# Kernel tuning notes

Measured on AMD Instinct MI355X. Metric: run time of the kernel, lower is better.

## Reference

```python
import jax, jax.numpy as jnp
import numpy as np

EPS = 1e-6
NUM_HEADS = 12


def ln_cf(x, w, b):
    # channels_first LayerNorm over channel dim (ConvNeXt style)
    u = jnp.mean(x, axis=1, keepdims=True)
    s = jnp.mean((x - u) ** 2, axis=1, keepdims=True)
    xn = (x - u) / jnp.sqrt(s + EPS)
    shp = (1, -1) + (1,) * (x.ndim - 2)
    return xn * w.reshape(shp) + b.reshape(shp)


def conv2s2(x, w):
    # Conv3d kernel=2 stride=2 (no bias): exact non-overlapping patch contraction
    b, c, H, W, D = x.shape
    xp = x.reshape(b, c, H // 2, 2, W // 2, 2, D // 2, 2)
    return jnp.einsum('bchkwpdq,ockpq->bohwd', xp, w)


def convt2s2(x, w):
    # ConvTranspose3d kernel=2 stride=2 (torch weight layout [in, out, 2,2,2])
    b, i, H, W, D = x.shape
    o = w.shape[1]
    y = jnp.einsum('bihwd,iokpq->bohkwpdq', x, w)
    return y.reshape(b, o, 2 * H, 2 * W, 2 * D)


def stem(x, w1, g1, b1, w2, g2, b2):
    h = conv2s2(x, w1)
    h = jax.nn.gelu(ln_cf(h, g1, b1), approximate=False)
    h = conv2s2(h, w2)
    return ln_cf(h, g2, b2)


def debed(x, tw1, g, b, tw2, tb2):
    h = convt2s2(x, tw1)
    h = jax.nn.gelu(ln_cf(h, g, b), approximate=False)
    return convt2s2(h, tw2) + tb2.reshape(1, -1, 1, 1, 1)


def rope(x):
    # rotary embedding over full token dim c (pairs (i, i+c/2)), positions 0..L-1
    b, l, c = x.shape
    inv = 1.0 / (10000.0 ** (jnp.arange(0, c, 2, dtype=jnp.float32) / c))
    t = jnp.arange(l, dtype=jnp.float32)
    f = jnp.outer(t, inv)                      # [l, c/2]
    emb = jnp.concatenate([f, f], axis=-1)     # [l, c]
    cos, sin = jnp.cos(emb)[None], jnp.sin(emb)[None]
    rot = jnp.concatenate([-x[..., c // 2:], x[..., :c // 2]], axis=-1)
    return x * cos + rot * sin


def _forward(x, skip, q_w1, q_g1, q_b1, q_w2, q_g2, q_b2,
             k_w1, k_g1, k_b1, k_w2, k_g2, k_b2,
             v_w1, v_g1, v_b1, v_w2, v_g2, v_b2,
             o_tw1, o_g, o_b, o_tw2, o_tb2,
             ns_w, ns_b, nx_w, nx_b, no_w, no_b):
    res = skip
    skip = ln_cf(skip, ns_w, ns_b)
    x = ln_cf(x, nx_w, nx_b)
    q = stem(skip, q_w1, q_g1, q_b1, q_w2, q_g2, q_b2)
    k = stem(x, k_w1, k_g1, k_b1, k_w2, k_g2, k_b2)
    v = stem(x, v_w1, v_g1, v_b1, v_w2, v_g2, v_b2)
    b, c, Hq, Wq, Dq = q.shape
    _, _, Hk, Wk, Dk = k.shape
    q = q.reshape(b, c, -1).transpose(0, 2, 1)   # [b, Lq, c]
    k = k.reshape(b, c, -1).transpose(0, 2, 1)   # [b, Lk, c]
    v = v.reshape(b, c, -1).transpose(0, 2, 1)
    q = rope(q)
    k = rope(k)
    hd = c // NUM_HEADS
    qh = q.reshape(b, -1, NUM_HEADS, hd).transpose(0, 2, 1, 3)  # [b, nh, Lq, hd]
    kh = k.reshape(b, -1, NUM_HEADS, hd).transpose(0, 2, 1, 3)
    vh = v.reshape(b, -1, NUM_HEADS, hd).transpose(0, 2, 1, 3)
    scale = 1.0 / jnp.sqrt(jnp.float32(hd))
    attn = jax.nn.softmax(jnp.einsum('bhqc,bhkc->bhqk', qh, kh) * scale, axis=-1)
    proj = jnp.einsum('bhqk,bhkc->bhqc', attn, vh)              # [b, nh, Lq, hd]
    # rearrange 'b nh l c -> b (c nh) h w d'
    proj = proj.transpose(0, 3, 1, 2).reshape(b, c, Hq, Wq, Dq)
    proj = ln_cf(proj, no_w, no_b)
    out = debed(proj, o_tw1, o_g, o_b, o_tw2, o_tb2)
    return out + res


def setup_inputs() -> dict:
    key = jax.random.key(0)
    ks = iter(jax.random.split(key, 40))
    def nrm(shape, scale):
        return jax.random.normal(next(ks), shape, jnp.float32) * scale
    E, E4, XF, SF = 768, 192, 6, 6
    inp = {
        'x': nrm((2, XF, 48, 48, 48), 1.0),
        'skip': nrm((2, SF, 48, 48, 48), 1.0),
    }
    for p, ic in [('q', SF), ('k', XF), ('v', XF)]:
        inp[p + '_w1'] = nrm((E4, ic, 2, 2, 2), (ic * 8) ** -0.5)
        inp[p + '_g1'] = jnp.ones(E4, jnp.float32)
        inp[p + '_b1'] = jnp.zeros(E4, jnp.float32)
        inp[p + '_w2'] = nrm((E, E4, 2, 2, 2), (E4 * 8) ** -0.5)
        inp[p + '_g2'] = jnp.ones(E, jnp.float32)
        inp[p + '_b2'] = jnp.zeros(E, jnp.float32)
    inp['o_tw1'] = nrm((E, E4, 2, 2, 2), E ** -0.5)
    inp['o_g'] = jnp.ones(E4, jnp.float32)
    inp['o_b'] = jnp.zeros(E4, jnp.float32)
    inp['o_tw2'] = nrm((E4, SF, 2, 2, 2), E4 ** -0.5)
    inp['o_tb2'] = jnp.zeros(SF, jnp.float32)
    inp['ns_w'] = jnp.ones(SF, jnp.float32)
    inp['ns_b'] = jnp.zeros(SF, jnp.float32)
    inp['nx_w'] = jnp.ones(XF, jnp.float32)
    inp['nx_b'] = jnp.zeros(XF, jnp.float32)
    inp['no_w'] = jnp.ones(E, jnp.float32)
    inp['no_b'] = jnp.zeros(E, jnp.float32)
    return inp


def reference(x, skip, q_w1, q_g1, q_b1, q_w2, q_g2, q_b2,
              k_w1, k_g1, k_b1, k_w2, k_g2, k_b2,
              v_w1, v_g1, v_b1, v_w2, v_g2, v_b2,
              o_tw1, o_g, o_b, o_tw2, o_tb2,
              ns_w, ns_b, nx_w, nx_b, no_w, no_b):
    return _forward(x, skip, q_w1, q_g1, q_b1, q_w2, q_g2, q_b2,
                    k_w1, k_g1, k_b1, k_w2, k_g2, k_b2,
                    v_w1, v_g1, v_b1, v_w2, v_g2, v_b2,
                    o_tw1, o_g, o_b, o_tw2, o_tb2,
                    ns_w, ns_b, nx_w, nx_b, no_w, no_b)
```

## Files before the change

### kernel.cpp

```cpp
#include <hip/hip_runtime.h>
#include <math.h>

#define BB_ 2
#define C0 6
#define S0 48
#define V0 (S0*S0*S0)
#define C1 192
#define S1 24
#define V1 (S1*S1*S1)
#define C2 768
#define S2 12
#define LL (S2*S2*S2)
#define NH 12
#define HD 64
#define KDIM (C1*8)
#define MDIM (BB_*LL)

typedef __attribute__((ext_vector_type(8))) short short8;
typedef __attribute__((ext_vector_type(4))) short short4v;
typedef __attribute__((ext_vector_type(4))) float float4v;

static __device__ __forceinline__ float gelu_exact(float x){
  return 0.5f*x*(1.0f+erff(x*0.70710678118654752440f));
}
static __device__ __forceinline__ unsigned short f2bf(float f){
  unsigned int u = __float_as_uint(f);
  unsigned int r = (u + 0x7fffu + ((u>>16)&1u)) >> 16;
  return (unsigned short)r;
}
static __device__ __forceinline__ unsigned int pk_bf16(float a, float b){
#if __has_builtin(__builtin_amdgcn_cvt_pk_bf16_f32)
  typedef __attribute__((ext_vector_type(2))) __bf16 bf2;
  bf2 r = __builtin_amdgcn_cvt_pk_bf16_f32(a,b);
  union { bf2 v; unsigned int u; } cv; cv.v = r;
  return cv.u;
#else
  return (unsigned int)f2bf(a) | ((unsigned int)f2bf(b)<<16);
#endif
}
static __device__ __forceinline__ float bf2f(unsigned short u){
  return __uint_as_float(((unsigned int)u)<<16);
}
static __device__ __forceinline__ void load_lds16(const void* g, void* l){
  __builtin_amdgcn_global_load_lds((const __attribute__((address_space(1))) unsigned int*)g,
      (__attribute__((address_space(3))) unsigned int*)l, 16, 0, 0);
}
static __device__ __forceinline__ float4v mfma32(short8 a, short8 b, float4v c){
  return __builtin_amdgcn_mfma_f32_16x16x32_bf16(a,b,c,0,0,0);
}
static __device__ __forceinline__ float4v mfma16(short4v a, short4v b, float4v c){
#if __has_builtin(__builtin_amdgcn_mfma_f32_16x16x16bf16_1k)
  return __builtin_amdgcn_mfma_f32_16x16x16bf16_1k(a,b,c,0,0,0);
#else
  asm volatile("v_mfma_f32_16x16x16_bf16 %0, %1, %2, %0" : "+v"(c) : "v"(a), "v"(b));
  return c;
#endif
}

__global__ __launch_bounds__(256) void prep_kernel(
    const float* __restrict__ skin, const float* __restrict__ xin,
    const float* __restrict__ nsw, const float* __restrict__ nsb,
    const float* __restrict__ nxw, const float* __restrict__ nxb,
    unsigned short* __restrict__ outS, unsigned short* __restrict__ outX,
    const float* __restrict__ qw2, const float* __restrict__ kw2, const float* __restrict__ vw2,
    const float* __restrict__ tw1, const float* __restrict__ tw2,
    unsigned short* __restrict__ w2tq, unsigned short* __restrict__ w2tk,
    unsigned short* __restrict__ w2tv, unsigned short* __restrict__ Btd,
    unsigned short* __restrict__ Bt48){
  int bx = blockIdx.x;
  if (bx < 1728){
    int z = bx >= 864;
    const float* in = z ? xin : skin;
    const float* w  = z ? nxw : nsw;
    const float* bi = z ? nxb : nsb;
    unsigned short* out = z ? outX : outS;
    int idx = (bx - z*864)*256 + threadIdx.x;
    int b = idx / V0, vox = idx - b*V0;
    const float* p = in + (size_t)b*(C0*V0) + vox;
    float v[C0]; float s=0.f;
#pragma unroll
    for (int c=0;c<C0;c++){ v[c]=p[(size_t)c*V0]; s+=v[c]; }
    float u = s*(1.f/C0);
    float ss=0.f;
#pragma unroll
    for (int c=0;c<C0;c++){ float d=v[c]-u; ss+=d*d; }
    float inv = rsqrtf(ss*(1.f/C0)+1e-6f);
    unsigned short* o = out + (size_t)b*(C0*V0) + vox;
#pragma unroll
    for (int c=0;c<C0;c++) o[(size_t)c*V0] = f2bf((v[c]-u)*inv*w[c]+bi[c]);
    return;
  }
  bx -= 1728;
  if (bx < 13824){
    int z = bx/4608;
    int idx = (bx - z*4608)*256 + threadIdx.x;
    const float* w2 = (z==0)?qw2:((z==1)?kw2:vw2);
    unsigned short* o = (z==0)?w2tq:((z==1)?w2tk:w2tv);
    int oc = idx/KDIM; int r = idx-oc*KDIM; int p = r/C1; int ic = r-p*C1;
    o[idx] = f2bf(w2[(size_t)oc*KDIM + ic*8 + p]);
  } else if (bx < 18432){
    int idx = (bx-13824)*256 + threadIdx.x;
    int n = idx/C2; int p = idx-n*C2;
    int i = ((p&63)*NH) + (p>>6);
    int kpq = n/C1, o2 = n-kpq*C1;
    Btd[idx] = f2bf(tw1[(size_t)i*KDIM + o2*8 + kpq]);
  } else {
    int idx = (bx-18432)*256 + threadIdx.x;
    int n = idx/C1; int i = idx-n*C1;
    Bt48[idx] = (n<48) ? f2bf(tw2[(size_t)i*48 + n]) : (unsigned short)0;
  }
}

__global__ __launch_bounds__(256) void conv1_kernel(
    const unsigned short* __restrict__ lnSb, const unsigned short* __restrict__ lnXb,
    const float* __restrict__ qw1, const float* __restrict__ qg1, const float* __restrict__ qb1,
    const float* __restrict__ kw1, const float* __restrict__ kg1, const float* __restrict__ kb1,
    const float* __restrict__ vw1, const float* __restrict__ vg1, const float* __restrict__ vb1,
    unsigned short* __restrict__ h1q, unsigned short* __restrict__ h1k,
    unsigned short* __restrict__ h1v){
  int z = blockIdx.z;
  const unsigned short* in = (z==0)? lnSb : lnXb;
  const float* w1 = (z==0)?qw1:((z==1)?kw1:vw1);
  const float* g1 = (z==0)?qg1:((z==1)?kg1:vg1);
  const float* b1 = (z==0)?qb1:((z==1)?kb1:vb1);
  unsigned short* h1p = (z==0)?h1q:((z==1)?h1k:h1v);
  __shared__ unsigned short Wl[C1*56];
  __shared__ float Gl[C1], Bl2[C1];
  int t = threadIdx.x, w = t>>6, lane = t&63;
  int g = lane>>4, l16 = lane&15;
  int j = blockIdx.x*4 + w;
  int bxh = j/18, mt = j - bxh*18;
  int b = bxh/48; int rem = bxh - b*48; int y = rem>>1, xh = rem&1;
  int xo = mt/3, zo = mt - xo*3;
  int xv = xh*12 + xo*2 + (l16>>3);
  int zv = zo*8 + (l16&7);
  int x2 = 2*xv, z2 = 2*zv, y2 = 2*y;
  const unsigned short* base = in + (size_t)b*C0*V0;
  union { short8 v; unsigned int u[4]; } aA;
  {
    size_t rb = (size_t)g*V0;
    aA.u[0] = *(const unsigned int*)&base[rb + (y2+0)*(S0*S0) + (x2+0)*S0 + z2];
    aA.u[1] = *(const unsigned int*)&base[rb + (y2+0)*(S0*S0) + (x2+1)*S0 + z2];
    aA.u[2] = *(const unsigned int*)&base[rb + (y2+1)*(S0*S0) + (x2+0)*S0 + z2];
    aA.u[3] = *(const unsigned int*)&base[rb + (y2+1)*(S0*S0) + (x2+1)*S0 + z2];
  }
  union { short4v v; unsigned int u[2]; } aB;
  {
    size_t rb = (size_t)(4+(g>>1))*V0 + (y2+(g&1))*(S0*S0);
    aB.u[0] = *(const unsigned int*)&base[rb + (x2+0)*S0 + z2];
    aB.u[1] = *(const unsigned int*)&base[rb + (x2+1)*S0 + z2];
  }
  for (int i4 = t; i4 < 2304; i4 += 256){
    int oc = i4/12, kk4 = (i4 - oc*12)*4;
    float4 f4 = *(const float4*)&w1[oc*48 + kk4];
    uint2 pk; pk.x = pk_bf16(f4.x,f4.y); pk.y = pk_bf16(f4.z,f4.w);
    *(uint2*)&Wl[oc*56 + kk4] = pk;
  }
  if (t < C1){ Gl[t] = g1[t]; Bl2[t] = b1[t]; }
  __syncthreads();
  float4v acc[12];
#pragma unroll
  for (int ot=0; ot<12; ot++){
    short8  wA = *(const short8*)&Wl[(ot*16+l16)*56 + g*8];
    short4v wB = *(const short4v*)&Wl[(ot*16+l16)*56 + 32 + g*4];
    float4v a = {};
    a = mfma32(wA, aA.v, a);
    a = mfma16(wB, aB.v, a);
    acc[ot] = a;
  }
  float s1=0.f, s2=0.f;
#pragma unroll
  for (int ot=0;ot<12;ot++)
#pragma unroll
    for (int reg=0;reg<4;reg++){ float v=acc[ot][reg]; s1+=v; s2+=v*v; }
  s1 += __shfl_xor(s1,16); s1 += __shfl_xor(s1,32);
  s2 += __shfl_xor(s2,16); s2 += __shfl_xor(s2,32);
  float u = s1*(1.f/C1);
  float inv = rsqrtf(s2*(1.f/C1)-u*u+1e-6f);
  int tok = (y>>1)*(S2*S2) + (xv>>1)*S2 + (zv>>1);
  int p8 = (y&1)*4 + (xv&1)*2 + (zv&1);
  unsigned short* hb = h1p + (size_t)(b*LL+tok)*KDIM + p8*C1;
#pragma unroll
  for (int ot=0; ot<12; ot++){
    int oc0 = ot*16 + g*4;
    float4 gg = *(const float4*)&Gl[oc0];
    float4 bb = *(const float4*)&Bl2[oc0];
    float x0 = gelu_exact((acc[ot][0]-u)*inv*gg.x+bb.x);
    float x1 = gelu_exact((acc[ot][1]-u)*inv*gg.y+bb.y);
    float x2e= gelu_exact((acc[ot][2]-u)*inv*gg.z+bb.z);
    float x3 = gelu_exact((acc[ot][3]-u)*inv*gg.w+bb.w);
    uint2 pk; pk.x = pk_bf16(x0,x1); pk.y = pk_bf16(x2e,x3);
    *(uint2*)&hb[oc0] = pk;
  }
}

__global__ __launch_bounds__(256) void gemm_stem_kernel(
    const unsigned short* __restrict__ A0, const unsigned short* __restrict__ A1,
    const unsigned short* __restrict__ A2,
    const unsigned short* __restrict__ B0, const unsigned short* __restrict__ B1,
    const unsigned short* __restrict__ B2,
    unsigned short* __restrict__ Cq, unsigned short* __restrict__ Ck,
    unsigned short* __restrict__ Cv){
  int flat = blockIdx.x;
  int xcd = flat & 7, slot = flat >> 3;
  int tile = xcd*61 + slot;
  if (tile >= 486) return;
  int z = tile/162; int rr = tile - z*162;
  int m0 = (rr/6)*128, n0 = (rr - (rr/6)*6)*128;
  const unsigned short* A = (z==0)?A0:((z==1)?A1:A2);
  const unsigned short* Bt = (z==0)?B0:((z==1)?B1:B2);
  unsigned short* Cp = (z==0)?Cq:((z==1)?Ck:Cv);
  __shared__ __align__(16) unsigned short Al[128*32];
  __shared__ __align__(16) unsigned short Bl[128*32];
  int t=threadIdx.x, w=t>>6, lane=t&63;
  int g=lane>>4, l16=lane&15, r16=lane>>2, c16=lane&3;
  int wm=w>>1, wn=w&1;
  float4v acc[4][4] = {};
  for (int kb=0;kb<KDIM;kb+=32){
    __syncthreads();
#pragma unroll
    for (int cc=0;cc<4;cc++){
      int ch = w*4+cc;
      if (ch<8){
        const unsigned short* gp = A + (size_t)(m0+ch*16+r16)*KDIM + kb + c16*8;
        load_lds16(gp, &Al[ch*512]);
      } else {
        const unsigned short* gp = Bt + (size_t)(n0+(ch-8)*16+r16)*KDIM + kb + c16*8;
        load_lds16(gp, &Bl[(ch-8)*512]);
      }
    }
    __syncthreads();
    short8 af[4], bf[4];
#pragma unroll
    for (int mt=0;mt<4;mt++) af[mt] = *(const short8*)&Al[(wm*64+mt*16+l16)*32 + g*8];
#pragma unroll
    for (int nt=0;nt<4;nt++) bf[nt] = *(const short8*)&Bl[(wn*64+nt*16+l16)*32 + g*8];
#pragma unroll
    for (int mt=0;mt<4;mt++)
#pragma unroll
      for (int nt=0;nt<4;nt++)
        acc[mt][nt] = mfma32(af[mt], bf[nt], acc[mt][nt]);
  }
#pragma unroll
  for (int mt=0;mt<4;mt++){
    int mb = m0 + wm*64 + mt*16 + g*4;
#pragma unroll
    for (int nt=0;nt<4;nt++){
      int col = n0 + wn*64 + nt*16 + l16;
#pragma unroll
      for (int reg=0;reg<4;reg++)
        Cp[(size_t)(mb+reg)*C2 + col] = f2bf(acc[mt][nt][reg]);
    }
  }
}

__global__ __launch_bounds__(256) void gemm_debed_kernel(const unsigned short* __restrict__ A,
    const unsigned short* __restrict__ Bt, unsigned short* __restrict__ C){
  int flat = blockIdx.x;
  int xcd = flat & 7, slot = flat >> 3;
  int tile = xcd*41 + slot;
  if (tile >= 324) return;
  int m0 = (tile/12)*128, n0 = (tile - (tile/12)*12)*128;
  __shared__ __align__(16) unsigned short Al[128*32];
  __shared__ __align__(16) unsigned short Bl[128*32];
  int t=threadIdx.x, w=t>>6, lane=t&63;
  int g=lane>>4, l16=lane&15, r16=lane>>2, c16=lane&3;
  int wm=w>>1, wn=w&1;
  float4v acc[4][4] = {};
  for (int kb=0;kb<C2;kb+=32){
    __syncthreads();
#pragma unroll
    for (int cc=0;cc<4;cc++){
      int ch = w*4+cc;
      if (ch<8){
        const unsigned short* gp = A + (size_t)(m0+ch*16+r16)*C2 + kb + c16*8;
        load_lds16(gp, &Al[ch*512]);
      } else {
        const unsigned short* gp = Bt + (size_t)(n0+(ch-8)*16+r16)*C2 + kb + c16*8;
        load_lds16(gp, &Bl[(ch-8)*512]);
      }
    }
    __syncthreads();
    short8 af[4], bf[4];
#pragma unroll
    for (int mt=0;mt<4;mt++) af[mt] = *(const short8*)&Al[(wm*64+mt*16+l16)*32 + g*8];
#pragma unroll
    for (int nt=0;nt<4;nt++) bf[nt] = *(const short8*)&Bl[(wn*64+nt*16+l16)*32 + g*8];
#pragma unroll
    for (int mt=0;mt<4;mt++)
#pragma unroll
      for (int nt=0;nt<4;nt++)
        acc[mt][nt] = mfma32(af[mt], bf[nt], acc[mt][nt]);
  }
#pragma unroll
  for (int nt=0;nt<4;nt++){
    int n = n0 + wn*64 + nt*16 + l16;
    int kpq = n / C1;
    int o = n - kpq*C1;
#pragma unroll
    for (int mt=0;mt<4;mt++){
      int mb = m0 + wm*64 + mt*16 + g*4;
#pragma unroll
      for (int reg=0;reg<4;reg++){
        int m = mb + reg;
        int b = m / LL; int tok = m - b*LL;
        int h = tok/(S2*S2), ww=(tok/S2)%S2, d=tok%S2;
        int v24 = (2*h+((kpq>>2)&1))*(S1*S1) + (2*ww+((kpq>>1)&1))*S1 + (2*d+(kpq&1));
        C[(size_t)(b*V1+v24)*C1 + o] = f2bf(acc[mt][nt][reg]);
      }
    }
  }
}

__global__ __launch_bounds__(256) void final_kernel(const unsigned short* __restrict__ dh,
    const unsigned short* __restrict__ Bt48, const float* __restrict__ og,
    const float* __restrict__ ob, const float* __restrict__ tb2s,
    const float* __restrict__ skipp, float* __restrict__ out){
  __shared__ __align__(16) unsigned short As[64*200];
  __shared__ __align__(16) unsigned short Bs[64*200];
  int t=threadIdx.x, w=t>>6, lane=t&63;
  int g=lane>>4, l16=lane&15;
  int m0 = blockIdx.x*64;
  for (int n8 = t; n8 < 1536; n8 += 256){
    int n64 = n8/24, kk = (n8 - n64*24)*8;
    uint4 d4 = *(const uint4*)&Bt48[n64*192 + kk];
    *(uint4*)&Bs[n64*200 + kk] = d4;
  }
  float g0=og[lane], g1v=og[lane+64], g2v=og[lane+128];
  float b0=ob[lane], b1v=ob[lane+64], b2v=ob[lane+128];
  for (int rr=0; rr<16; rr++){
    int rl = w*16 + rr;
    const unsigned short* row = dh + (size_t)(m0+rl)*C1;
    float v0=bf2f(row[lane]), v1=bf2f(row[lane+64]), v2=bf2f(row[lane+128]);
    float s1=v0+v1+v2, s2=v0*v0+v1*v1+v2*v2;
#pragma unroll
    for (int off=32;off>0;off>>=1){ s1+=__shfl_xor(s1,off); s2+=__shfl_xor(s2,off); }
    float u=s1*(1.f/C1), inv=rsqrtf(s2*(1.f/C1)-u*u+1e-6f);
    As[rl*200+lane]     = f2bf(gelu_exact((v0-u)*inv*g0+b0));
    As[rl*200+lane+64]  = f2bf(gelu_exact((v1-u)*inv*g1v+b1v));
    As[rl*200+lane+128] = f2bf(gelu_exact((v2-u)*inv*g2v+b2v));
  }
  __syncthreads();
  int wm=w>>1, wn=w&1;
  float4v acc[2][2] = {};
#pragma unroll
  for (int kb=0;kb<192;kb+=32){
    short8 af[2], bf[2];
#pragma unroll
    for (int mt=0;mt<2;mt++) af[mt] = *(const short8*)&As[(wm*32+mt*16+l16)*200 + kb + g*8];
#pragma unroll
    for (int nt=0;nt<2;nt++) bf[nt] = *(const short8*)&Bs[(wn*32+nt*16+l16)*200 + kb + g*8];
#pragma unroll
    for (int mt=0;mt<2;mt++)
#pragma unroll
      for (int nt=0;nt<2;nt++)
        acc[mt][nt] = mfma32(af[mt], bf[nt], acc[mt][nt]);
  }
#pragma unroll
  for (int nt=0;nt<2;nt++){
    int n = wn*32 + nt*16 + l16;
    if (n < 48){
      int c = n>>3, kpq = n&7;
      float bias = tb2s[c];
#pragma unroll
      for (int mt=0;mt<2;mt++){
        int mb = m0 + wm*32 + mt*16 + g*4;
#pragma unroll
        for (int reg=0;reg<4;reg++){
          int m = mb + reg;
          int b = m / V1; int v24 = m - b*V1;
          int y24 = v24/(S1*S1), x24=(v24/S1)%S1, z24=v24%S1;
          int vox = (2*y24+((kpq>>2)&1))*(S0*S0) + (2*x24+((kpq>>1)&1))*S0 + 2*z24+(kpq&1);
          size_t oi = (size_t)(b*C0+c)*V0 + vox;
          out[oi] = acc[mt][nt][reg] + bias + skipp[oi];
        }
      }
    }
  }
}

__global__ __launch_bounds__(64) void ln768_stem_kernel(
    unsigned short* __restrict__ qb, unsigned short* __restrict__ kb2,
    unsigned short* __restrict__ vb,
    const float* __restrict__ qg, const float* __restrict__ qbi,
    const float* __restrict__ kg, const float* __restrict__ kbi,
    const float* __restrict__ vg, const float* __restrict__ vbi, float qscale){
  int z = blockIdx.y;
  unsigned short* buf = (z==0)?qb:((z==1)?kb2:vb);
  const float* g  = (z==0)?qg:((z==1)?kg:vg);
  const float* bia= (z==0)?qbi:((z==1)?kbi:vbi);
  float scale = (z==0)? qscale : 1.0f;
  int tok = blockIdx.x, lane = threadIdx.x;
  unsigned short* row = buf + (size_t)tok*C2;
  float v[12]; float s1=0.f,s2=0.f;
#pragma unroll
  for (int i=0;i<12;i++){ float t=bf2f(row[i*64+lane]); v[i]=t; s1+=t; s2+=t*t; }
#pragma unroll
  for (int off=32;off>0;off>>=1){ s1+=__shfl_xor(s1,off); s2+=__shfl_xor(s2,off); }
  float u=s1*(1.f/C2);
  float inv=rsqrtf(s2*(1.f/C2)-u*u+1e-6f);
  if (z==2){
#pragma unroll
    for (int i=0;i<12;i++){ int j=i*64+lane; row[j]=f2bf((v[i]-u)*inv*g[j]+bia[j]); }
  } else {
    int pos = tok % LL;
#pragma unroll
    for (int i=0;i<6;i++){
      int j=i*64+lane;
      float xn1=(v[i]-u)*inv*g[j]+bia[j];
      float xn2=(v[i+6]-u)*inv*g[j+384]+bia[j+384];
      float fr=(float)pos*__expf(-0.02398526139f*(float)j);
      float cs=cosf(fr), sn=sinf(fr);
      row[j]     = f2bf((xn1*cs - xn2*sn)*scale);
      row[j+384] = f2bf((xn2*cs + xn1*sn)*scale);
    }
  }
}

__global__ __launch_bounds__(256) void vtrans_kernel(const unsigned short* __restrict__ vbf,
    unsigned short* __restrict__ vT){
  int idx = blockIdx.x*256 + threadIdx.x;
  int token = idx % LL;
  int rest = idx / LL;
  int dc = rest & 7;
  int hb = rest >> 3;
  int h = hb % NH, b = hb / NH;
  const unsigned short* src = vbf + (size_t)(b*LL+token)*C2 + h*64 + dc*8;
  uint4 d4 = *(const uint4*)src;
  const unsigned short* s = (const unsigned short*)&d4;
#pragma unroll
  for (int i=0;i<8;i++)
    vT[(size_t)((b*NH+h)*HD + dc*8 + i)*LL + token] = s[i];
}

__global__ __launch_bounds__(256) void attn_kernel(const unsigned short* __restrict__ q,
    const unsigned short* __restrict__ k, const unsigned short* __restrict__ vt,
    unsigned short* __restrict__ opart, float* __restrict__ lbuf){
  __shared__ __align__(16) unsigned char smem[18432];
  unsigned short* Ks = (unsigned short*)smem;
  unsigned short* Vs = Ks + 4096;
  int qt=blockIdx.x, h=blockIdx.y;
  int b = blockIdx.z>>2, split = blockIdx.z&3;
  int t=threadIdx.x, w=t>>6, lane=t&63;
  int g=lane>>4, l16=lane&15;
  const unsigned short* qrow = q + (size_t)(b*LL + qt*64 + w*16 + l16)*C2 + h*64;
  short8 qA = *(const short8*)(qrow + g*8);
  short8 qB = *(const short8*)(qrow + 32 + g*8);
  const unsigned short* kbase = k + (size_t)(b*LL)*C2 + h*64;
  const unsigned short* vbase = vt + (size_t)((b*NH+h)*HD)*LL;
  int sub = lane>>3;
  int chs = (lane&7) ^ sub;
  float lrow = 0.f;
  float4v O4[4] = {};
  int ktb = split*7, kte = (split==3)? 27 : (split*7+7);
  for (int kt=ktb; kt<kte; kt++){
    __syncthreads();
#pragma unroll
    for (int cc=0;cc<4;cc++){
      int ii = w*4+cc;
      if (ii<8){
        int key = kt*64 + ii*8 + sub;
        load_lds16(kbase + (size_t)key*C2 + chs*8, &Ks[ii*512]);
      } else {
        int d = (ii-8)*8 + sub;
        load_lds16(vbase + (size_t)d*LL + kt*64 + chs*8, &Vs[(ii-8)*512]);
      }
    }
    __syncthreads();
    float4v sc[4];
#pragma unroll
    for (int nt=0;nt<4;nt++){
      int row = nt*16 + l16;
      int sw = row & 7;
      short8 k1 = *(const short8*)&Ks[row*64 + ((g^sw))*8];
      short8 k2 = *(const short8*)&Ks[row*64 + (((4+g)^sw))*8];
      float4v z = {};
      z = mfma32(k1, qA, z);
      z = mfma32(k2, qB, z);
      sc[nt] = z;
    }
#pragma unroll
    for (int nt=0;nt<4;nt++)
#pragma unroll
      for (int reg=0;reg<4;reg++){
        float e = exp2f(sc[nt][reg]); sc[nt][reg]=e; lrow+=e;
      }
#pragma unroll
    for (int kc=0;kc<4;kc++){
      union { short4v v; unsigned int u[2]; } pb;
      pb.u[0] = pk_bf16(sc[kc][0], sc[kc][1]);
      pb.u[1] = pk_bf16(sc[kc][2], sc[kc][3]);
#pragma unroll
      for (int dt=0;dt<4;dt++){
        int row = dt*16 + l16;
        int ch = (kc*2 + (g>>1)) ^ (row&7);
        short4v va = *(const short4v*)&Vs[row*64 + ch*8 + (g&1)*4];
        O4[dt] = mfma16(va, pb.v, O4[dt]);
      }
    }
  }
  lrow += __shfl_xor(lrow,16);
  lrow += __shfl_xor(lrow,32);
  __syncthreads();
  float* Ot = (float*)smem;
  float* ot = Ot + w*1152;
#pragma unroll
  for (int dt=0;dt<4;dt++)
    *(float4*)&ot[l16*72 + dt*16 + g*4] =
        make_float4(O4[dt][0],O4[dt][1],O4[dt][2],O4[dt][3]);
  if (g==0){
    int qi = qt*64 + w*16 + l16;
    lbuf[((size_t)(b*4+split)*NH+h)*LL + qi] = lrow;
  }
  int qq = lane>>2, c4 = lane&3;
  unsigned short* orow = opart + (size_t)split*MDIM*C2
              + (size_t)(b*LL + qt*64 + w*16 + qq)*C2 + h*64;
#pragma unroll
  for (int p=0;p<4;p++){
    float4 vv = *(float4*)&ot[qq*72 + p*16 + c4*4];
    uint2 pk; pk.x = pk_bf16(vv.x,vv.y); pk.y = pk_bf16(vv.z,vv.w);
    *(uint2*)&orow[p*16 + c4*4] = pk;
  }
}

__global__ __launch_bounds__(256) void attn_post_kernel(const unsigned short* __restrict__ opart,
    const float* __restrict__ lbuf,
    const float* __restrict__ g, const float* __restrict__ bia,
    unsigned short* __restrict__ aob){
  int t=threadIdx.x, w=t>>6, lane=t&63;
  int m = blockIdx.x*4 + w;
  int b = m / LL, l = m - b*LL;
  const unsigned short* o0 = opart + (size_t)m*C2;
  unsigned short* orow = aob + (size_t)m*C2;
  float vv[12]; float s1=0.f, s2=0.f;
#pragma unroll
  for (int i=0;i<12;i++){
    float ls = 0.f;
#pragma unroll
    for (int s=0;s<4;s++) ls += lbuf[((size_t)(b*4+s)*NH+i)*LL + l];
    float inv = 1.f/ls;
    int j = i*64+lane;
    float val = 0.f;
#pragma unroll
    for (int s=0;s<4;s++) val += bf2f(o0[(size_t)s*MDIM*C2 + j]);
    val *= inv;
    vv[i]=val; s1+=val; s2+=val*val;
  }
#pragma unroll
  for (int off=32;off>0;off>>=1){ s1+=__shfl_xor(s1,off); s2+=__shfl_xor(s2,off); }
  float u=s1*(1.f/C2);
  float invs=rsqrtf(s2*(1.f/C2)-u*u+1e-6f);
#pragma unroll
  for (int i=0;i<12;i++){
    int cj = lane*NH + i;
    orow[i*64+lane] = f2bf((vv[i]-u)*invs*g[cj]+bia[cj]);
  }
}

extern "C" void kernel_launch(void* const* d_in, const int* in_sizes, int n_in,
                              void* d_out, int out_size, void* d_ws, size_t ws_size,
                              hipStream_t stream){
  (void)in_sizes; (void)n_in; (void)out_size; (void)ws_size;
  const float* x    =(const float*)d_in[0];
  const float* skip =(const float*)d_in[1];
  const float* q_w1 =(const float*)d_in[2];
  const float* q_g1 =(const float*)d_in[3];
  const float* q_b1 =(const float*)d_in[4];
  const float* q_w2 =(const float*)d_in[5];
  const float* q_g2 =(const float*)d_in[6];
  const float* q_b2 =(const float*)d_in[7];
  const float* k_w1 =(const float*)d_in[8];
  const float* k_g1 =(const float*)d_in[9];
  const float* k_b1 =(const float*)d_in[10];
  const float* k_w2 =(const float*)d_in[11];
  const float* k_g2 =(const float*)d_in[12];
  const float* k_b2 =(const float*)d_in[13];
  const float* v_w1 =(const float*)d_in[14];
  const float* v_g1 =(const float*)d_in[15];
  const float* v_b1 =(const float*)d_in[16];
  const float* v_w2 =(const float*)d_in[17];
  const float* v_g2 =(const float*)d_in[18];
  const float* v_b2 =(const float*)d_in[19];
  const float* o_tw1=(const float*)d_in[20];
  const float* o_g  =(const float*)d_in[21];
  const float* o_b  =(const float*)d_in[22];
  const float* o_tw2=(const float*)d_in[23];
  const float* o_tb2=(const float*)d_in[24];
  const float* ns_w =(const float*)d_in[25];
  const float* ns_b =(const float*)d_in[26];
  const float* nx_w =(const float*)d_in[27];
  const float* nx_b =(const float*)d_in[28];
  const float* no_w =(const float*)d_in[29];
  const float* no_b =(const float*)d_in[30];
  float* out=(float*)d_out;

  char* W = (char*)d_ws;
  unsigned short* lnSb = (unsigned short*)(W + 0);
  unsigned short* lnXb = (unsigned short*)(W + 2654208);
  unsigned short* h1q  = (unsigned short*)(W + 5308416);
  unsigned short* h1k  = (unsigned short*)(W + 15925248);
  unsigned short* h1v  = (unsigned short*)(W + 26542080);
  unsigned short* w2tq = (unsigned short*)(W + 37158912);
  unsigned short* w2tk = (unsigned short*)(W + 39518208);
  unsigned short* w2tv = (unsigned short*)(W + 41877504);
  unsigned short* qbf  = (unsigned short*)(W + 44236800);
  unsigned short* kbf  = (unsigned short*)(W + 49545216);
  unsigned short* vbf  = (unsigned short*)(W + 54853632);
  unsigned short* vT   = (unsigned short*)(W + 60162048);
  unsigned short* aob  = (unsigned short*)(W + 65470464);
  unsigned short* Btd  = (unsigned short*)(W + 70778880);
  unsigned short* Bt48 = (unsigned short*)(W + 73138176);
  float* lbuf  = (float*)(W + 0);
  unsigned short* opart = (unsigned short*)(W + 5308416);
  unsigned short* dh   = (unsigned short*)(W + 5308416);

  const float QSCALE = 0.125f*1.44269504089f;

  prep_kernel<<<20208,256,0,stream>>>(skip, x, ns_w, ns_b, nx_w, nx_b, lnSb, lnXb,
      q_w2,k_w2,v_w2,o_tw1,o_tw2, w2tq,w2tk,w2tv,Btd,Bt48);
  conv1_kernel<<<dim3(432,1,3),256,0,stream>>>(lnSb,lnXb,
      q_w1,q_g1,q_b1, k_w1,k_g1,k_b1, v_w1,v_g1,v_b1, h1q,h1k,h1v);
  gemm_stem_kernel<<<488,256,0,stream>>>(h1q,h1k,h1v,
      w2tq,w2tk,w2tv, qbf,kbf,vbf);
  ln768_stem_kernel<<<dim3(MDIM,3),64,0,stream>>>(qbf,kbf,vbf,
      q_g2,q_b2, k_g2,k_b2, v_g2,v_b2, QSCALE);
  vtrans_kernel<<<1296,256,0,stream>>>(vbf, vT);
  attn_kernel<<<dim3(27,12,8),256,0,stream>>>(qbf, kbf, vT, opart, lbuf);
  attn_post_kernel<<<864,256,0,stream>>>(opart, lbuf, no_w, no_b, aob);
  gemm_debed_kernel<<<328,256,0,stream>>>(aob, Btd, dh);
  final_kernel<<<432,256,0,stream>>>(dh, Bt48, o_g, o_b, o_tb2, skip, out);
}
```

Before: 334.8 us.

## Pre-convert conv1 weights in prep, XCD-remap attention grid, MFMA row sums

Conv1 weights are now converted to bf16 once in the prep kernel, and conv1 reads them and the LN params straight from global memory, which drops the shared-memory staging and its barrier. The attention grid is flattened and remapped so tiles sharing a head land on the same XCD, aiming for better L2 reuse of K/V. The softmax row sum is computed by an extra MFMA against a ones vector instead of per-element adds and shuffles, taking the work off the VALU. The trade-offs are uncached global weight loads in conv1 and a row sum built from bf16-rounded probabilities.

Result: no change. 329.0 us (-1.7%).

```diff
diff --git a/kernel.cpp b/kernel.cpp
--- a/kernel.cpp
+++ b/kernel.cpp
@@ -64,9 +64,12 @@
     unsigned short* __restrict__ outS, unsigned short* __restrict__ outX,
     const float* __restrict__ qw2, const float* __restrict__ kw2, const float* __restrict__ vw2,
     const float* __restrict__ tw1, const float* __restrict__ tw2,
+    const float* __restrict__ qw1, const float* __restrict__ kw1, const float* __restrict__ vw1,
     unsigned short* __restrict__ w2tq, unsigned short* __restrict__ w2tk,
     unsigned short* __restrict__ w2tv, unsigned short* __restrict__ Btd,
-    unsigned short* __restrict__ Bt48){
+    unsigned short* __restrict__ Bt48,
+    unsigned short* __restrict__ w1q, unsigned short* __restrict__ w1k,
+    unsigned short* __restrict__ w1v){
   int bx = blockIdx.x;
   if (bx < 1728){
     int z = bx >= 864;
@@ -104,28 +107,34 @@
     int i = ((p&63)*NH) + (p>>6);
     int kpq = n/C1, o2 = n-kpq*C1;
     Btd[idx] = f2bf(tw1[(size_t)i*KDIM + o2*8 + kpq]);
-  } else {
+  } else if (bx < 18480){
     int idx = (bx-18432)*256 + threadIdx.x;
     int n = idx/C1; int i = idx-n*C1;
     Bt48[idx] = (n<48) ? f2bf(tw2[(size_t)i*48 + n]) : (unsigned short)0;
+  } else {
+    int idx = (bx-18480)*256 + threadIdx.x;
+    int z = idx / 9216; int r = idx - z*9216;
+    const float* w1 = (z==0)?qw1:((z==1)?kw1:vw1);
+    unsigned short* o = (z==0)?w1q:((z==1)?w1k:w1v);
+    o[r] = f2bf(w1[r]);
   }
 }
 
 __global__ __launch_bounds__(256) void conv1_kernel(
     const unsigned short* __restrict__ lnSb, const unsigned short* __restrict__ lnXb,
-    const float* __restrict__ qw1, const float* __restrict__ qg1, const float* __restrict__ qb1,
-    const float* __restrict__ kw1, const float* __restrict__ kg1, const float* __restrict__ kb1,
-    const float* __restrict__ vw1, const float* __restrict__ vg1, const float* __restrict__ vb1,
+    const unsigned short* __restrict__ w1bq, const unsigned short* __restrict__ w1bk,
+    const unsigned short* __restrict__ w1bv,
+    const float* __restrict__ qg1, const float* __restrict__ qb1,
+    const float* __restrict__ kg1, const float* __restrict__ kb1,
+    const float* __restrict__ vg1, const float* __restrict__ vb1,
     unsigned short* __restrict__ h1q, unsigned short* __restrict__ h1k,
     unsigned short* __restrict__ h1v){
   int z = blockIdx.z;
   const unsigned short* in = (z==0)? lnSb : lnXb;
-  const float* w1 = (z==0)?qw1:((z==1)?kw1:vw1);
+  const unsigned short* Wb = (z==0)?w1bq:((z==1)?w1bk:w1bv);
   const float* g1 = (z==0)?qg1:((z==1)?kg1:vg1);
   const float* b1 = (z==0)?qb1:((z==1)?kb1:vb1);
   unsigned short* h1p = (z==0)?h1q:((z==1)?h1k:h1v);
-  __shared__ unsigned short Wl[C1*56];
-  __shared__ float Gl[C1], Bl2[C1];
   int t = threadIdx.x, w = t>>6, lane = t&63;
   int g = lane>>4, l16 = lane&15;
   int j = blockIdx.x*4 + w;
@@ -150,19 +159,11 @@
     aB.u[0] = *(const unsigned int*)&base[rb + (x2+0)*S0 + z2];
     aB.u[1] = *(const unsigned int*)&base[rb + (x2+1)*S0 + z2];
   }
-  for (int i4 = t; i4 < 2304; i4 += 256){
-    int oc = i4/12, kk4 = (i4 - oc*12)*4;
-    float4 f4 = *(const float4*)&w1[oc*48 + kk4];
-    uint2 pk; pk.x = pk_bf16(f4.x,f4.y); pk.y = pk_bf16(f4.z,f4.w);
-    *(uint2*)&Wl[oc*56 + kk4] = pk;
-  }
-  if (t < C1){ Gl[t] = g1[t]; Bl2[t] = b1[t]; }
-  __syncthreads();
   float4v acc[12];
 #pragma unroll
   for (int ot=0; ot<12; ot++){
-    short8  wA = *(const short8*)&Wl[(ot*16+l16)*56 + g*8];
-    short4v wB = *(const short4v*)&Wl[(ot*16+l16)*56 + 32 + g*4];
+    short8  wA = *(const short8*)&Wb[(ot*16+l16)*48 + g*8];
+    short4v wB = *(const short4v*)&Wb[(ot*16+l16)*48 + 32 + g*4];
     float4v a = {};
     a = mfma32(wA, aA.v, a);
     a = mfma16(wB, aB.v, a);
@@ -183,8 +184,8 @@
 #pragma unroll
   for (int ot=0; ot<12; ot++){
     int oc0 = ot*16 + g*4;
-    float4 gg = *(const float4*)&Gl[oc0];
-    float4 bb = *(const float4*)&Bl2[oc0];
+    float4 gg = *(const float4*)&g1[oc0];
+    float4 bb = *(const float4*)&b1[oc0];
     float x0 = gelu_exact((acc[ot][0]-u)*inv*gg.x+bb.x);
     float x1 = gelu_exact((acc[ot][1]-u)*inv*gg.y+bb.y);
     float x2e= gelu_exact((acc[ot][2]-u)*inv*gg.z+bb.z);
@@ -439,8 +440,12 @@
   __shared__ __align__(16) unsigned char smem[18432];
   unsigned short* Ks = (unsigned short*)smem;
   unsigned short* Vs = Ks + 4096;
-  int qt=blockIdx.x, h=blockIdx.y;
-  int b = blockIdx.z>>2, split = blockIdx.z&3;
+  int flat = blockIdx.x;
+  int xcd = flat & 7, slot = flat >> 3;
+  int tile = xcd*324 + slot;
+  int h = tile / 216; int rem = tile - h*216;
+  int zb = rem / 27, qt = rem - zb*27;
+  int b = zb >> 2, split = zb & 3;
   int t=threadIdx.x, w=t>>6, lane=t&63;
   int g=lane>>4, l16=lane&15;
   const unsigned short* qrow = q + (size_t)(b*LL + qt*64 + w*16 + l16)*C2 + h*64;
@@ -450,8 +455,10 @@
   const unsigned short* vbase = vt + (size_t)((b*NH+h)*HD)*LL;
   int sub = lane>>3;
   int chs = (lane&7) ^ sub;
-  float lrow = 0.f;
+  short4v vones;
+  vones[0]=vones[1]=vones[2]=vones[3]=(short)0x3F80;
   float4v O4[4] = {};
+  float4v Ol = {};
   int ktb = split*7, kte = (split==3)? 27 : (split*7+7);
   for (int kt=ktb; kt<kte; kt++){
     __syncthreads();
@@ -482,14 +489,14 @@
 #pragma unroll
     for (int nt=0;nt<4;nt++)
 #pragma unroll
-      for (int reg=0;reg<4;reg++){
-        float e = exp2f(sc[nt][reg]); sc[nt][reg]=e; lrow+=e;
-      }
+      for (int reg=0;reg<4;reg++)
+        sc[nt][reg] = exp2f(sc[nt][reg]);
 #pragma unroll
     for (int kc=0;kc<4;kc++){
       union { short4v v; unsigned int u[2]; } pb;
       pb.u[0] = pk_bf16(sc[kc][0], sc[kc][1]);
       pb.u[1] = pk_bf16(sc[kc][2], sc[kc][3]);
+      Ol = mfma16(vones, pb.v, Ol);
 #pragma unroll
       for (int dt=0;dt<4;dt++){
         int row = dt*16 + l16;
@@ -499,8 +506,6 @@
       }
     }
   }
-  lrow += __shfl_xor(lrow,16);
-  lrow += __shfl_xor(lrow,32);
   __syncthreads();
   float* Ot = (float*)smem;
   float* ot = Ot + w*1152;
@@ -510,7 +515,7 @@
         make_float4(O4[dt][0],O4[dt][1],O4[dt][2],O4[dt][3]);
   if (g==0){
     int qi = qt*64 + w*16 + l16;
-    lbuf[((size_t)(b*4+split)*NH+h)*LL + qi] = lrow;
+    lbuf[((size_t)(b*4+split)*NH+h)*LL + qi] = Ol[0];
   }
   int qq = lane>>2, c4 = lane&3;
   unsigned short* orow = opart + (size_t)split*MDIM*C2
@@ -610,22 +615,26 @@
   unsigned short* aob  = (unsigned short*)(W + 65470464);
   unsigned short* Btd  = (unsigned short*)(W + 70778880);
   unsigned short* Bt48 = (unsigned short*)(W + 73138176);
+  unsigned short* w1q  = (unsigned short*)(W + 73162752);
+  unsigned short* w1k  = (unsigned short*)(W + 73181184);
+  unsigned short* w1v  = (unsigned short*)(W + 73199616);
   float* lbuf  = (float*)(W + 0);
   unsigned short* opart = (unsigned short*)(W + 5308416);
   unsigned short* dh   = (unsigned short*)(W + 5308416);
 
   const float QSCALE = 0.125f*1.44269504089f;
 
-  prep_kernel<<<20208,256,0,stream>>>(skip, x, ns_w, ns_b, nx_w, nx_b, lnSb, lnXb,
-      q_w2,k_w2,v_w2,o_tw1,o_tw2, w2tq,w2tk,w2tv,Btd,Bt48);
-  conv1_kernel<<<dim3(432,1,3),256,0,stream>>>(lnSb,lnXb,
-      q_w1,q_g1,q_b1, k_w1,k_g1,k_b1, v_w1,v_g1,v_b1, h1q,h1k,h1v);
+  prep_kernel<<<20316,256,0,stream>>>(skip, x, ns_w, ns_b, nx_w, nx_b, lnSb, lnXb,
+      q_w2,k_w2,v_w2,o_tw1,o_tw2, q_w1,k_w1,v_w1,
+      w2tq,w2tk,w2tv,Btd,Bt48, w1q,w1k,w1v);
+  conv1_kernel<<<dim3(432,1,3),256,0,stream>>>(lnSb,lnXb, w1q,w1k,w1v,
+      q_g1,q_b1, k_g1,k_b1, v_g1,v_b1, h1q,h1k,h1v);
   gemm_stem_kernel<<<488,256,0,stream>>>(h1q,h1k,h1v,
       w2tq,w2tk,w2tv, qbf,kbf,vbf);
   ln768_stem_kernel<<<dim3(MDIM,3),64,0,stream>>>(qbf,kbf,vbf,
       q_g2,q_b2, k_g2,k_b2, v_g2,v_b2, QSCALE);
   vtrans_kernel<<<1296,256,0,stream>>>(vbf, vT);
-  attn_kernel<<<dim3(27,12,8),256,0,stream>>>(qbf, kbf, vT, opart, lbuf);
+  attn_kernel<<<2592,256,0,stream>>>(qbf, kbf, vT, opart, lbuf);
   attn_post_kernel<<<864,256,0,stream>>>(opart, lbuf, no_w, no_b, aob);
   gemm_debed_kernel<<<328,256,0,stream>>>(aob, Btd, dh);
   final_kernel<<<432,256,0,stream>>>(dh, Bt48, o_g, o_b, o_tb2, skip, out);
```
